# Kernel optimization log

Measured on AMD Instinct MI355X. Metric: run time of the kernel, lower is better.

Reference implementation:

```python
import jax, jax.numpy as jnp
import numpy as np

NUM_LEVELS = 8
NODES_PER_LEVEL = 16384
CHILDREN_PER_NODE = 8
DIM = 64


def _build_layered_dag():
    rng = np.random.default_rng(0)
    srcs, dsts = [], []
    for lvl in range(NUM_LEVELS - 1):
        child_base = lvl * NODES_PER_LEVEL
        parent_base = (lvl + 1) * NODES_PER_LEVEL
        children = rng.integers(0, NODES_PER_LEVEL, size=(NODES_PER_LEVEL, CHILDREN_PER_NODE)) + child_base
        parents = np.repeat(np.arange(NODES_PER_LEVEL) + parent_base, CHILDREN_PER_NODE)
        srcs.append(children.ravel())
        dsts.append(parents)
    ei = np.stack([np.concatenate(srcs), np.concatenate(dsts)]).astype(np.int32)
    return jnp.asarray(ei)


def setup_inputs() -> dict:
    key = jax.random.key(0)
    k1, k2, k3, k4 = jax.random.split(key, 4)
    N = NUM_LEVELS * NODES_PER_LEVEL
    x = jax.random.normal(k1, (N, DIM), dtype=jnp.float32)
    edge_index = _build_layered_dag()
    s = 1.0 / np.sqrt(DIM)
    W_l = jax.random.uniform(k2, (DIM, DIM), jnp.float32, -s, s)
    b_l = jax.random.uniform(k3, (DIM,), jnp.float32, -s, s)
    W_r = jax.random.uniform(k4, (DIM, DIM), jnp.float32, -s, s)
    return {"x": x, "edge_index": edge_index, "W_l": W_l, "b_l": b_l,
            "W_r": W_r, "num_levels": NUM_LEVELS}


def reference(x, edge_index, W_l, b_l, W_r, num_levels):
    N, d = x.shape
    src, dst = edge_index[0], edge_index[1]
    E = src.shape[0]

    # in-degree; leaves have no incoming edges
    indeg = jax.ops.segment_sum(jnp.ones((E,), jnp.int32), dst, num_segments=N)
    leaves = indeg == 0                                   # [N] bool

    out = jnp.where(leaves[:, None], jnp.tanh(x), 0.0)    # out[leaves] = tanh(x[leaves])
    visited = leaves

    # root_weight path: overwrite rows of out where x row is nonzero
    row_nonzero = jnp.any(x != 0, axis=1)
    out = jnp.where(row_nonzero[:, None], x @ W_r.T, out)

    prev = leaves  # previous_visits as boolean node mask
    for _ in range(num_levels - 1):
        mask_e = prev[src]                                # edges from previous front
        acv = jax.ops.segment_sum((visited[src] & mask_e).astype(jnp.int32), dst, num_segments=N)
        tc = jax.ops.segment_sum(mask_e.astype(jnp.int32), dst, num_segments=N)
        fathers = tc > 0
        ref_next = fathers & (acv == tc)                  # parents with all children visited

        m2 = ref_next[dst]
        agg = jax.ops.segment_sum(jnp.where(m2[:, None], out[src], 0.0), dst, num_segments=N)
        upd = agg @ W_l.T + b_l
        out = jnp.where(ref_next[:, None], jnp.tanh(out + upd), out)
        visited = visited | ref_next
        prev = ref_next
    return out
```

## Files before the change

kernel.cpp:

```cpp
#include <hip/hip_runtime.h>

#define NPL   16384
#define DIM   64
#define CPN   8
#define EPL   (NPL * CPN)
#define NLEV  8

#define TPB     512
#define WPB     (TPB / 64)
#define CBLOCKS 256
#define NPB     (NPL / CBLOCKS)
#define NPW     (NPB / WPB)

__device__ __forceinline__ float co_ld(const float* p) {
    return __hip_atomic_load(p, __ATOMIC_RELAXED, __HIP_MEMORY_SCOPE_AGENT);
}
__device__ __forceinline__ void co_st(float* p, float v) {
    __hip_atomic_store(p, v, __ATOMIC_RELAXED, __HIP_MEMORY_SCOPE_AGENT);
}

__device__ __forceinline__ void load_wrow(float* dst, const float* W, int row) {
    const float4* p = (const float4*)(W + row * DIM);
    #pragma unroll
    for (int q = 0; q < DIM / 4; ++q) {
        float4 v = p[q];
        dst[4*q+0] = v.x; dst[4*q+1] = v.y;
        dst[4*q+2] = v.z; dst[4*q+3] = v.w;
    }
}

__device__ __forceinline__ float fast_tanh(float z) {
    z = fminf(15.f, fmaxf(-15.f, z));
    float e = __expf(-2.f * z);
    return (1.f - e) * __builtin_amdgcn_rcpf(1.f + e);
}

__device__ __forceinline__ void gridbar(int* cnt, int target) {
    __syncthreads();
    if (threadIdx.x == 0) {
        __hip_atomic_fetch_add(cnt, 1, __ATOMIC_RELAXED,
                               __HIP_MEMORY_SCOPE_AGENT);
        while (__hip_atomic_load(cnt, __ATOMIC_RELAXED,
                                 __HIP_MEMORY_SCOPE_AGENT) < target)
            __builtin_amdgcn_s_sleep(8);
    }
    asm volatile("" ::: "memory");
    __syncthreads();
}

template<bool COH>
__device__ __forceinline__ void phaseA(
    const float* __restrict__ x, const float* __restrict__ Wr,
    float* __restrict__ out, float* __restrict__ XR,
    int lane, int w, int blk, float* sX4 )
{
    float wr[DIM];
    load_wrow(wr, Wr, lane);

    const int base = blk * NPB + w * NPW;
    const int sub  = lane >> 4;
    const int col4 = (lane & 15) * 4;

    float4 q0, q1, q2;
    #define ROWB(g) ((long)((g) >> 1) * NPL + base + ((g) & 1) * 4)
    q0 = *(const float4*)&x[(ROWB(0) + sub) * DIM + col4];
    q1 = *(const float4*)&x[(ROWB(1) + sub) * DIM + col4];

    for (int g = 0; g < 16; ++g) {
        if (g + 2 < 16)
            q2 = *(const float4*)&x[(ROWB(g + 2) + sub) * DIM + col4];

        *(float4*)&sX4[sub * DIM + col4] = q0;

        const long rb = ROWB(g);
        const int  L  = g >> 1;
        #pragma unroll
        for (int rr = 0; rr < 4; ++rr) {
            float a0 = 0.f, a1 = 0.f, a2 = 0.f, a3 = 0.f;
            const float4* A = (const float4*)&sX4[rr * DIM];
            #pragma unroll
            for (int k = 0; k < DIM / 4; ++k) {
                float4 av = A[k];
                a0 += av.x * wr[4*k+0];
                a1 += av.y * wr[4*k+1];
                a2 += av.z * wr[4*k+2];
                a3 += av.w * wr[4*k+3];
            }
            float r = (a0 + a1) + (a2 + a3);
            const long gg = rb + rr;
            if (L == 0) {
                float* d = &out[gg * DIM + lane];
                if (COH) co_st(d, r); else *d = r;
            } else {
                XR[gg * DIM + lane] = r;
            }
        }
        q0 = q1; q1 = q2;
    }
    #undef ROWB
}

template<bool COH>
__device__ __forceinline__ void phaseB(
    const int* __restrict__ eb,
    const float* __restrict__ XR, float* __restrict__ out,
    const float* wl, float bias,
    int L, int lane, int w, int blk, float* sA )
{
    const int  pbase = blk * NPB + w * NPW;
    const long gbase = (long)L * NPL;

    const int vidx = eb[pbase * CPN + lane];

    float g0[CPN], g1[CPN], g2[CPN];
    float xr0, xr1, xr2;

    #define ISSUE(c, gg, xr)                                                  \
        {                                                                     \
            _Pragma("unroll")                                                 \
            for (int j = 0; j < CPN; ++j) {                                   \
                int s = __builtin_amdgcn_readlane(vidx, (c) * CPN + j);       \
                const float* p = &out[(long)s * DIM + lane];                  \
                gg[j] = COH ? co_ld(p) : *p;                                  \
            }                                                                 \
            xr = XR[(gbase + pbase + (c)) * DIM + lane];                      \
        }

    ISSUE(0, g0, xr0);
    ISSUE(1, g1, xr1);

    #pragma unroll
    for (int c = 0; c < NPW; ++c) {
        if (c + 2 < NPW) ISSUE(c + 2, g2, xr2);

        float agg = 0.f;
        #pragma unroll
        for (int j = 0; j < CPN; ++j) agg += g0[j];
        sA[lane] = agg;

        float a0 = 0.f, a1 = 0.f, a2 = 0.f, a3 = bias + xr0;
        const float4* B = (const float4*)sA;
        #pragma unroll
        for (int k = 0; k < DIM / 4; ++k) {
            float4 bv = B[k];
            a0 += bv.x * wl[4*k+0];
            a1 += bv.y * wl[4*k+1];
            a2 += bv.z * wl[4*k+2];
            a3 += bv.w * wl[4*k+3];
        }
        float r = fast_tanh((a0 + a1) + (a2 + a3));
        float* d = &out[(gbase + pbase + c) * DIM + lane];
        if (COH) co_st(d, r); else *d = r;

        #pragma unroll
        for (int j = 0; j < CPN; ++j) { g0[j] = g1[j]; g1[j] = g2[j]; }
        xr0 = xr1; xr1 = xr2;
    }
    #undef ISSUE
}

__global__ __launch_bounds__(TPB, 2) void dag_fused(
    const float* __restrict__ x, const int* __restrict__ src,
    const float* __restrict__ Wl, const float* __restrict__ bl,
    const float* __restrict__ Wr, float* __restrict__ out,
    float* __restrict__ ws)
{
    __shared__ __align__(16) float sbuf[WPB][256];

    const int lane = threadIdx.x & 63;
    const int w    = threadIdx.x >> 6;

    int*   barcnt = (int*)ws;
    float* XR     = ws + 64;

    phaseA<true>(x, Wr, out, XR, lane, w, blockIdx.x, sbuf[w]);
    gridbar(barcnt, CBLOCKS);

    float wl[DIM];
    load_wrow(wl, Wl, lane);
    const float bias = bl[lane];

    for (int L = 1; L < NLEV; ++L) {
        phaseB<true>(src + (long)(L - 1) * EPL, XR, out, wl, bias,
                     L, lane, w, blockIdx.x, sbuf[w]);
        if (L + 1 < NLEV)
            gridbar(barcnt, (L + 1) * CBLOCKS);
    }
}

__global__ __launch_bounds__(TPB) void dag_phaseA_k(
    const float* __restrict__ x, const float* __restrict__ Wr,
    float* __restrict__ out, float* __restrict__ ws)
{
    __shared__ __align__(16) float sbuf[WPB][256];
    const int lane = threadIdx.x & 63;
    const int w    = threadIdx.x >> 6;
    phaseA<false>(x, Wr, out, ws + 64, lane, w, blockIdx.x, sbuf[w]);
}

__global__ __launch_bounds__(TPB) void dag_phaseB_k(
    const int* __restrict__ src, const float* __restrict__ Wl,
    const float* __restrict__ bl, float* __restrict__ out,
    float* __restrict__ ws, int L)
{
    __shared__ __align__(16) float sbuf[WPB][256];
    const int lane = threadIdx.x & 63;
    const int w    = threadIdx.x >> 6;
    float wl[DIM];
    load_wrow(wl, Wl, lane);
    phaseB<false>(src + (long)(L - 1) * EPL, ws + 64, out, wl, bl[lane],
                  L, lane, w, blockIdx.x, sbuf[w]);
}

extern "C" void kernel_launch(void* const* d_in, const int* in_sizes, int n_in,
                              void* d_out, int out_size, void* d_ws, size_t ws_size,
                              hipStream_t stream) {
    const float* x  = (const float*)d_in[0];
    const int*   ei = (const int*)d_in[1];
    const float* Wl = (const float*)d_in[2];
    const float* bl = (const float*)d_in[3];
    const float* Wr = (const float*)d_in[4];
    float* out = (float*)d_out;
    float* ws  = (float*)d_ws;

    const int* src = ei;

    hipMemsetAsync(ws, 0, 256, stream);

    void* args[] = {(void*)&x, (void*)&src, (void*)&Wl, (void*)&bl,
                    (void*)&Wr, (void*)&out, (void*)&ws};
    hipError_t e = hipLaunchCooperativeKernel((const void*)dag_fused,
                                              dim3(CBLOCKS), dim3(TPB),
                                              args, 0, stream);
    if (e != hipSuccess) {
        (void)hipGetLastError();
        hipLaunchKernelGGL(dag_phaseA_k, dim3(CBLOCKS), dim3(TPB), 0, stream,
                           x, Wr, out, ws);
        for (int L = 1; L < NLEV; ++L) {
            hipLaunchKernelGGL(dag_phaseB_k, dim3(CBLOCKS), dim3(TPB), 0, stream,
                               src, Wl, bl, out, ws, L);
        }
    }
}
```

Before: 226.1 us.

## Double cooperative grid size, drop XR scratch, and preload edge indices upfront

Templates the fused cooperative kernel on block count and launches 512 blocks with launch bounds allowing four blocks per CU, falling back to 256 and then to separate kernels. The x@W_r^T result for non-leaf levels is now written straight into out instead of an XR scratch buffer, and phaseB reads it back from out. All per-level child index loads are hoisted before phaseA, and the barrier spin sleep is shortened. This aims for more parallelism per level and less latency exposed at grid barriers, at the cost of more blocks taking part in each barrier and tighter register limits under the higher occupancy bound.

Result: slower. 319.6 us (+41.4%).

```diff
diff --git a/kernel.cpp b/kernel.cpp
--- a/kernel.cpp
+++ b/kernel.cpp
@@ -6,11 +6,8 @@
 #define EPL   (NPL * CPN)
 #define NLEV  8
 
-#define TPB     512
-#define WPB     (TPB / 64)
-#define CBLOCKS 256
-#define NPB     (NPL / CBLOCKS)
-#define NPW     (NPB / WPB)
+#define TPB   512
+#define WPB   (TPB / 64)
 
 __device__ __forceinline__ float co_ld(const float* p) {
     return __hip_atomic_load(p, __ATOMIC_RELAXED, __HIP_MEMORY_SCOPE_AGENT);
@@ -42,18 +39,22 @@
                                __HIP_MEMORY_SCOPE_AGENT);
         while (__hip_atomic_load(cnt, __ATOMIC_RELAXED,
                                  __HIP_MEMORY_SCOPE_AGENT) < target)
-            __builtin_amdgcn_s_sleep(8);
+            __builtin_amdgcn_s_sleep(2);
     }
     asm volatile("" ::: "memory");
     __syncthreads();
 }
 
-template<bool COH>
+template<int CB, bool COH>
 __device__ __forceinline__ void phaseA(
     const float* __restrict__ x, const float* __restrict__ Wr,
-    float* __restrict__ out, float* __restrict__ XR,
-    int lane, int w, int blk, float* sX4 )
-{
+    float* __restrict__ out, int lane, int w, int blk, float* sX4)
+{
+    constexpr int NPB = NPL / CB;
+    constexpr int NPW = NPB / WPB;
+    constexpr int GPL = NPW / 4;
+    constexpr int NG  = NLEV * GPL;
+
     float wr[DIM];
     load_wrow(wr, Wr, lane);
 
@@ -62,18 +63,18 @@
     const int col4 = (lane & 15) * 4;
 
     float4 q0, q1, q2;
-    #define ROWB(g) ((long)((g) >> 1) * NPL + base + ((g) & 1) * 4)
+    #define ROWB(g) ((long)((g) / GPL) * NPL + base + ((g) % GPL) * 4)
     q0 = *(const float4*)&x[(ROWB(0) + sub) * DIM + col4];
-    q1 = *(const float4*)&x[(ROWB(1) + sub) * DIM + col4];
-
-    for (int g = 0; g < 16; ++g) {
-        if (g + 2 < 16)
+    if (NG > 1) q1 = *(const float4*)&x[(ROWB(1) + sub) * DIM + col4];
+
+    #pragma unroll
+    for (int g = 0; g < NG; ++g) {
+        if (g + 2 < NG)
             q2 = *(const float4*)&x[(ROWB(g + 2) + sub) * DIM + col4];
 
         *(float4*)&sX4[sub * DIM + col4] = q0;
 
         const long rb = ROWB(g);
-        const int  L  = g >> 1;
         #pragma unroll
         for (int rr = 0; rr < 4; ++rr) {
             float a0 = 0.f, a1 = 0.f, a2 = 0.f, a3 = 0.f;
@@ -87,30 +88,23 @@
                 a3 += av.w * wr[4*k+3];
             }
             float r = (a0 + a1) + (a2 + a3);
-            const long gg = rb + rr;
-            if (L == 0) {
-                float* d = &out[gg * DIM + lane];
-                if (COH) co_st(d, r); else *d = r;
-            } else {
-                XR[gg * DIM + lane] = r;
-            }
+            float* d = &out[(rb + rr) * DIM + lane];
+            if (COH) co_st(d, r); else *d = r;
         }
         q0 = q1; q1 = q2;
     }
     #undef ROWB
 }
 
-template<bool COH>
+template<int CB, bool COH>
 __device__ __forceinline__ void phaseB(
-    const int* __restrict__ eb,
-    const float* __restrict__ XR, float* __restrict__ out,
-    const float* wl, float bias,
-    int L, int lane, int w, int blk, float* sA )
-{
+    int vidx, float* __restrict__ out,
+    const float* wl, float bias, int L, int lane, int w, int blk, float* sA)
+{
+    constexpr int NPB = NPL / CB;
+    constexpr int NPW = NPB / WPB;
     const int  pbase = blk * NPB + w * NPW;
     const long gbase = (long)L * NPL;
-
-    const int vidx = eb[pbase * CPN + lane];
 
     float g0[CPN], g1[CPN], g2[CPN];
     float xr0, xr1, xr2;
@@ -123,11 +117,14 @@
                 const float* p = &out[(long)s * DIM + lane];                  \
                 gg[j] = COH ? co_ld(p) : *p;                                  \
             }                                                                 \
-            xr = XR[(gbase + pbase + (c)) * DIM + lane];                      \
+            {                                                                 \
+                const float* p = &out[(gbase + pbase + (c)) * DIM + lane];    \
+                xr = COH ? co_ld(p) : *p;                                     \
+            }                                                                 \
         }
 
     ISSUE(0, g0, xr0);
-    ISSUE(1, g1, xr1);
+    if (NPW > 1) ISSUE(1, g1, xr1);
 
     #pragma unroll
     for (int c = 0; c < NPW; ++c) {
@@ -159,7 +156,8 @@
     #undef ISSUE
 }
 
-__global__ __launch_bounds__(TPB, 2) void dag_fused(
+template<int CB>
+__global__ __launch_bounds__(TPB, 4) void dag_fused(
     const float* __restrict__ x, const int* __restrict__ src,
     const float* __restrict__ Wl, const float* __restrict__ bl,
     const float* __restrict__ Wr, float* __restrict__ out,
@@ -167,49 +165,60 @@
 {
     __shared__ __align__(16) float sbuf[WPB][256];
 
+    constexpr int NPB  = NPL / CB;
+    constexpr int NPW  = NPB / WPB;
+    constexpr int NIDX = NPW * CPN;
+
     const int lane = threadIdx.x & 63;
     const int w    = threadIdx.x >> 6;
-
-    int*   barcnt = (int*)ws;
-    float* XR     = ws + 64;
-
-    phaseA<true>(x, Wr, out, XR, lane, w, blockIdx.x, sbuf[w]);
-    gridbar(barcnt, CBLOCKS);
+    int* barcnt = (int*)ws;
+
+    const int pbase = blockIdx.x * NPB + w * NPW;
+    int vidx[NLEV - 1];
+    #pragma unroll
+    for (int L = 1; L < NLEV; ++L)
+        vidx[L - 1] = src[(long)(L - 1) * EPL + pbase * CPN + (lane & (NIDX - 1))];
+
+    phaseA<CB, true>(x, Wr, out, lane, w, blockIdx.x, sbuf[w]);
+    gridbar(barcnt, CB);
 
     float wl[DIM];
     load_wrow(wl, Wl, lane);
     const float bias = bl[lane];
 
+    #pragma unroll
     for (int L = 1; L < NLEV; ++L) {
-        phaseB<true>(src + (long)(L - 1) * EPL, XR, out, wl, bias,
-                     L, lane, w, blockIdx.x, sbuf[w]);
+        phaseB<CB, true>(vidx[L - 1], out, wl, bias, L, lane, w,
+                         blockIdx.x, sbuf[w]);
         if (L + 1 < NLEV)
-            gridbar(barcnt, (L + 1) * CBLOCKS);
+            gridbar(barcnt, (L + 1) * CB);
     }
 }
 
 __global__ __launch_bounds__(TPB) void dag_phaseA_k(
     const float* __restrict__ x, const float* __restrict__ Wr,
-    float* __restrict__ out, float* __restrict__ ws)
+    float* __restrict__ out)
 {
     __shared__ __align__(16) float sbuf[WPB][256];
     const int lane = threadIdx.x & 63;
     const int w    = threadIdx.x >> 6;
-    phaseA<false>(x, Wr, out, ws + 64, lane, w, blockIdx.x, sbuf[w]);
+    phaseA<512, false>(x, Wr, out, lane, w, blockIdx.x, sbuf[w]);
 }
 
 __global__ __launch_bounds__(TPB) void dag_phaseB_k(
     const int* __restrict__ src, const float* __restrict__ Wl,
-    const float* __restrict__ bl, float* __restrict__ out,
-    float* __restrict__ ws, int L)
+    const float* __restrict__ bl, float* __restrict__ out, int L)
 {
     __shared__ __align__(16) float sbuf[WPB][256];
     const int lane = threadIdx.x & 63;
     const int w    = threadIdx.x >> 6;
+    constexpr int NPB = NPL / 512, NPW = NPB / WPB, NIDX = NPW * CPN;
+    const int pbase = blockIdx.x * NPB + w * NPW;
+    int vidx = src[(long)(L - 1) * EPL + pbase * CPN + (lane & (NIDX - 1))];
     float wl[DIM];
     load_wrow(wl, Wl, lane);
-    phaseB<false>(src + (long)(L - 1) * EPL, ws + 64, out, wl, bl[lane],
-                  L, lane, w, blockIdx.x, sbuf[w]);
+    phaseB<512, false>(vidx, out, wl, bl[lane], L, lane, w,
+                       blockIdx.x, sbuf[w]);
 }
 
 extern "C" void kernel_launch(void* const* d_in, const int* in_sizes, int n_in,
@@ -229,16 +238,22 @@
 
     void* args[] = {(void*)&x, (void*)&src, (void*)&Wl, (void*)&bl,
                     (void*)&Wr, (void*)&out, (void*)&ws};
-    hipError_t e = hipLaunchCooperativeKernel((const void*)dag_fused,
-                                              dim3(CBLOCKS), dim3(TPB),
+
+    hipError_t e = hipLaunchCooperativeKernel((const void*)dag_fused<512>,
+                                              dim3(512), dim3(TPB),
                                               args, 0, stream);
     if (e != hipSuccess) {
         (void)hipGetLastError();
-        hipLaunchKernelGGL(dag_phaseA_k, dim3(CBLOCKS), dim3(TPB), 0, stream,
-                           x, Wr, out, ws);
+        e = hipLaunchCooperativeKernel((const void*)dag_fused<256>,
+                                       dim3(256), dim3(TPB), args, 0, stream);
+    }
+    if (e != hipSuccess) {
+        (void)hipGetLastError();
+        hipLaunchKernelGGL(dag_phaseA_k, dim3(512), dim3(TPB), 0, stream,
+                           x, Wr, out);
         for (int L = 1; L < NLEV; ++L) {
-            hipLaunchKernelGGL(dag_phaseB_k, dim3(CBLOCKS), dim3(TPB), 0, stream,
-                               src, Wl, bl, out, ws, L);
-        }
-    }
-}
+            hipLaunchKernelGGL(dag_phaseB_k, dim3(512), dim3(TPB), 0, stream,
+                               src, Wl, bl, out, L);
+        }
+    }
+}
```

## Prefetch edge indices upfront, deepen gather pipeline, use plain loads, shorten barrier sleep

Applied to the files above, without the earlier changes.

Loads every level's child-index vector before phase A, so the per-level src read leaves the critical path after each grid barrier. Deepens the neighbour-gather prefetch from 2 to 3 chunks, using a rotating register slot array instead of shifting buffers. Replaces relaxed atomic loads of `out` with plain loads, fully unrolls phase A, and shortens the spin-wait sleep in the grid barrier. The costs are higher register pressure, and plain loads with no acquire fence after the barrier, which could read stale cached data across CUs.

After: 222.8 us. About the same (-1.5%).

```diff
diff --git a/kernel.cpp b/kernel.cpp
--- a/kernel.cpp
+++ b/kernel.cpp
@@ -12,9 +12,6 @@
 #define NPB     (NPL / CBLOCKS)
 #define NPW     (NPB / WPB)
 
-__device__ __forceinline__ float co_ld(const float* p) {
-    return __hip_atomic_load(p, __ATOMIC_RELAXED, __HIP_MEMORY_SCOPE_AGENT);
-}
 __device__ __forceinline__ void co_st(float* p, float v) {
     __hip_atomic_store(p, v, __ATOMIC_RELAXED, __HIP_MEMORY_SCOPE_AGENT);
 }
@@ -42,7 +39,7 @@
                                __HIP_MEMORY_SCOPE_AGENT);
         while (__hip_atomic_load(cnt, __ATOMIC_RELAXED,
                                  __HIP_MEMORY_SCOPE_AGENT) < target)
-            __builtin_amdgcn_s_sleep(8);
+            __builtin_amdgcn_s_sleep(2);
     }
     asm volatile("" ::: "memory");
     __syncthreads();
@@ -52,8 +49,11 @@
 __device__ __forceinline__ void phaseA(
     const float* __restrict__ x, const float* __restrict__ Wr,
     float* __restrict__ out, float* __restrict__ XR,
-    int lane, int w, int blk, float* sX4 )
-{
+    int lane, int w, int blk, float* sX4)
+{
+    constexpr int GPL = NPW / 4;
+    constexpr int NG  = NLEV * GPL;
+
     float wr[DIM];
     load_wrow(wr, Wr, lane);
 
@@ -62,18 +62,19 @@
     const int col4 = (lane & 15) * 4;
 
     float4 q0, q1, q2;
-    #define ROWB(g) ((long)((g) >> 1) * NPL + base + ((g) & 1) * 4)
+    #define ROWB(g) ((long)((g) / GPL) * NPL + base + ((g) % GPL) * 4)
     q0 = *(const float4*)&x[(ROWB(0) + sub) * DIM + col4];
     q1 = *(const float4*)&x[(ROWB(1) + sub) * DIM + col4];
 
-    for (int g = 0; g < 16; ++g) {
-        if (g + 2 < 16)
+    #pragma unroll
+    for (int g = 0; g < NG; ++g) {
+        if (g + 2 < NG)
             q2 = *(const float4*)&x[(ROWB(g + 2) + sub) * DIM + col4];
 
         *(float4*)&sX4[sub * DIM + col4] = q0;
 
         const long rb = ROWB(g);
-        const int  L  = g >> 1;
+        const int  L  = g / GPL;
         #pragma unroll
         for (int rr = 0; rr < 4; ++rr) {
             float a0 = 0.f, a1 = 0.f, a2 = 0.f, a3 = 0.f;
@@ -102,43 +103,42 @@
 
 template<bool COH>
 __device__ __forceinline__ void phaseB(
-    const int* __restrict__ eb,
-    const float* __restrict__ XR, float* __restrict__ out,
-    const float* wl, float bias,
-    int L, int lane, int w, int blk, float* sA )
+    int vidx, const float* __restrict__ XR, float* __restrict__ out,
+    const float* wl, float bias, int L, int lane, int w, int blk, float* sA)
 {
     const int  pbase = blk * NPB + w * NPW;
     const long gbase = (long)L * NPL;
 
-    const int vidx = eb[pbase * CPN + lane];
-
-    float g0[CPN], g1[CPN], g2[CPN];
-    float xr0, xr1, xr2;
-
-    #define ISSUE(c, gg, xr)                                                  \
+    float g[4][CPN];
+    float xr[4];
+
+    #define ISSUE(c, s)                                                       \
         {                                                                     \
             _Pragma("unroll")                                                 \
             for (int j = 0; j < CPN; ++j) {                                   \
-                int s = __builtin_amdgcn_readlane(vidx, (c) * CPN + j);       \
-                const float* p = &out[(long)s * DIM + lane];                  \
-                gg[j] = COH ? co_ld(p) : *p;                                  \
+                int si = __builtin_amdgcn_readlane(vidx, (c) * CPN + j);      \
+                g[s][j] = out[(long)si * DIM + lane];      \
             }                                                                 \
-            xr = XR[(gbase + pbase + (c)) * DIM + lane];                      \
-        }
-
-    ISSUE(0, g0, xr0);
-    ISSUE(1, g1, xr1);
+            xr[s] = XR[(gbase + pbase + (c)) * DIM + lane];                   \
+        }
+
+    ISSUE(0, 0);
+    ISSUE(1, 1);
+    ISSUE(2, 2);
 
     #pragma unroll
     for (int c = 0; c < NPW; ++c) {
-        if (c + 2 < NPW) ISSUE(c + 2, g2, xr2);
-
-        float agg = 0.f;
-        #pragma unroll
-        for (int j = 0; j < CPN; ++j) agg += g0[j];
+        const int slot = c & 3;
+        if (c + 3 < NPW) ISSUE(c + 3, (c + 3) & 3);
+
+        float s0 = g[slot][0] + g[slot][1];
+        float s1 = g[slot][2] + g[slot][3];
+        float s2 = g[slot][4] + g[slot][5];
+        float s3 = g[slot][6] + g[slot][7];
+        float agg = (s0 + s1) + (s2 + s3);
         sA[lane] = agg;
 
-        float a0 = 0.f, a1 = 0.f, a2 = 0.f, a3 = bias + xr0;
+        float a0 = 0.f, a1 = 0.f, a2 = 0.f, a3 = bias + xr[slot];
         const float4* B = (const float4*)sA;
         #pragma unroll
         for (int k = 0; k < DIM / 4; ++k) {
@@ -151,10 +151,6 @@
         float r = fast_tanh((a0 + a1) + (a2 + a3));
         float* d = &out[(gbase + pbase + c) * DIM + lane];
         if (COH) co_st(d, r); else *d = r;
-
-        #pragma unroll
-        for (int j = 0; j < CPN; ++j) { g0[j] = g1[j]; g1[j] = g2[j]; }
-        xr0 = xr1; xr1 = xr2;
     }
     #undef ISSUE
 }
@@ -173,6 +169,12 @@
     int*   barcnt = (int*)ws;
     float* XR     = ws + 64;
 
+    const int pbase = blockIdx.x * NPB + w * NPW;
+    int vidx[NLEV - 1];
+    #pragma unroll
+    for (int L = 1; L < NLEV; ++L)
+        vidx[L - 1] = src[(long)(L - 1) * EPL + pbase * CPN + lane];
+
     phaseA<true>(x, Wr, out, XR, lane, w, blockIdx.x, sbuf[w]);
     gridbar(barcnt, CBLOCKS);
 
@@ -180,9 +182,10 @@
     load_wrow(wl, Wl, lane);
     const float bias = bl[lane];
 
+    #pragma unroll
     for (int L = 1; L < NLEV; ++L) {
-        phaseB<true>(src + (long)(L - 1) * EPL, XR, out, wl, bias,
-                     L, lane, w, blockIdx.x, sbuf[w]);
+        phaseB<true>(vidx[L - 1], XR, out, wl, bias, L, lane, w,
+                     blockIdx.x, sbuf[w]);
         if (L + 1 < NLEV)
             gridbar(barcnt, (L + 1) * CBLOCKS);
     }
@@ -206,10 +209,12 @@
     __shared__ __align__(16) float sbuf[WPB][256];
     const int lane = threadIdx.x & 63;
     const int w    = threadIdx.x >> 6;
+    const int pbase = blockIdx.x * NPB + w * NPW;
+    int vidx = src[(long)(L - 1) * EPL + pbase * CPN + lane];
     float wl[DIM];
     load_wrow(wl, Wl, lane);
-    phaseB<false>(src + (long)(L - 1) * EPL, ws + 64, out, wl, bl[lane],
-                  L, lane, w, blockIdx.x, sbuf[w]);
+    phaseB<false>(vidx, ws + 64, out, wl, bl[lane], L, lane, w,
+                  blockIdx.x, sbuf[w]);
 }
 
 extern "C" void kernel_launch(void* const* d_in, const int* in_sizes, int n_in,
```
